# Kernel optimization log

Hardware: AMD Instinct MI355X
Metric: run time of the kernel (lower is better)

## Reference

```python
import jax, jax.numpy as jnp
import numpy as np

N_PTS0 = 32      # n_sampling_points
N_PTS1 = 8       # n_final_points after maxpool
DIM_LOI = 128    # hardcoded via reshape(128, ...) in LinePooling
DIM_FC = 1024
N_LABELS = 3
C_IN = 256
H = W = 128
N_LINES = 16000


def setup_inputs() -> dict:
    key = jax.random.key(0)
    ks = jax.random.split(key, 8)
    features = jax.random.normal(ks[0], (1, C_IN, H, W), jnp.float32)
    # line endpoints (x1,y1,x2,y2) in feature-map coordinates [0, 128)
    lines = jax.random.uniform(ks[1], (N_LINES, 4), jnp.float32) * 128.0
    w_fc1 = jax.random.normal(ks[2], (DIM_LOI, C_IN), jnp.float32) / np.sqrt(C_IN)
    b_fc1 = jnp.zeros((DIM_LOI,), jnp.float32)
    w1 = jax.random.normal(ks[3], (DIM_FC, DIM_LOI * N_PTS1), jnp.float32) / np.sqrt(DIM_LOI * N_PTS1)
    b1 = jnp.zeros((DIM_FC,), jnp.float32)
    w2 = jax.random.normal(ks[4], (DIM_FC, DIM_FC), jnp.float32) / np.sqrt(DIM_FC)
    b2 = jnp.zeros((DIM_FC,), jnp.float32)
    w3 = jax.random.normal(ks[5], (N_LABELS, DIM_FC), jnp.float32) / np.sqrt(DIM_FC)
    b3 = jnp.zeros((N_LABELS,), jnp.float32)
    return {"features": features, "lines": lines, "w_fc1": w_fc1, "b_fc1": b_fc1,
            "w1": w1, "b1": b1, "w2": w2, "b2": b2, "w3": w3, "b3": b3}


def _line_pool(loi, lines):
    # loi: [C, H, W]; lines: [N, 4] -> pooled features [N, C * N_PTS1]
    h, w = loi.shape[1], loi.shape[2]
    tspan = jnp.linspace(0.0, 1.0, N_PTS0)[None, None, :]          # [1,1,S]
    U, V = lines[:, :2], lines[:, 2:]                               # [N,2]
    pts = U[:, :, None] * tspan + V[:, :, None] * (1.0 - tspan) - 0.5  # [N,2,S]
    pts = pts.transpose(0, 2, 1).reshape(-1, 2)                     # [N*S,2]
    px, py = pts[:, 0], pts[:, 1]
    px0 = jnp.clip(jnp.floor(px), 0.0, w - 1)
    py0 = jnp.clip(jnp.floor(py), 0.0, h - 1)
    px1 = jnp.clip(px0 + 1.0, 0.0, w - 1)
    py1 = jnp.clip(py0 + 1.0, 0.0, h - 1)
    px0l, py0l = px0.astype(jnp.int32), py0.astype(jnp.int32)
    px1l, py1l = px1.astype(jnp.int32), py1.astype(jnp.int32)
    # four-corner bilinear gather: each gather is [C, N*S]
    xp = (loi[:, py0l, px0l] * (py1 - py) * (px1 - px)
          + loi[:, py1l, px0l] * (py - py0) * (px1 - px)
          + loi[:, py0l, px1l] * (py1 - py) * (px - px0)
          + loi[:, py1l, px1l] * (py - py0) * (px - px0))
    xp = xp.reshape(DIM_LOI, -1, N_PTS0).transpose(1, 0, 2)         # [N,C,S]
    k = N_PTS0 // N_PTS1
    xp = xp.reshape(xp.shape[0], DIM_LOI, N_PTS1, k).max(axis=-1)   # maxpool1d
    return xp.reshape(-1, N_PTS1 * DIM_LOI)                         # [N, C*P1]


def reference(features, lines, w_fc1, b_fc1, w1, b1, w2, b2, w3, b3):
    # fc1: 1x1 conv 256 -> 128 + ReLU (batch = 1)
    loi = jax.nn.relu(jnp.einsum('oc,chw->ohw', w_fc1, features[0]) + b_fc1[:, None, None])
    feat = _line_pool(loi, lines)                                   # [N, 1024]
    x = jax.nn.relu(feat @ w1.T + b1)
    x = jax.nn.relu(x @ w2.T + b2)
    logits = x @ w3.T + b3                                          # [N, N_LABELS]
    return logits
```

## Files before the change

### kernel.cpp

```cpp
#include <hip/hip_runtime.h>
#include <hip/hip_bf16.h>
#include <math.h>

#define C_IN 256
#define HW 128
#define NPIX (HW*HW)
#define DIM_LOI 128
#define N_LINES 16000
#define N_PTS0 32
#define N_PTS1 8
#define DIM_FC 1024
#define N_LABELS 3

typedef __attribute__((ext_vector_type(8))) short short8;
typedef __attribute__((ext_vector_type(4))) float f32x4;

__global__ __launch_bounds__(256) void transpose_feats(
    const float* __restrict__ feats,
    __hip_bfloat16* __restrict__ featsT)
{
    __shared__ float tile[64][65];
    const int t = threadIdx.x;
    const int p0 = blockIdx.x * 64;
    const int c0 = blockIdx.y * 64;
#pragma unroll
    for (int i = 0; i < 4; ++i) {
        int c = (t >> 4) + i * 16;
        int p4 = (t & 15) * 4;
        float4 v = *(const float4*)(feats + (size_t)(c0 + c) * NPIX + p0 + p4);
        tile[c][p4 + 0] = v.x;
        tile[c][p4 + 1] = v.y;
        tile[c][p4 + 2] = v.z;
        tile[c][p4 + 3] = v.w;
    }
    __syncthreads();
#pragma unroll
    for (int i = 0; i < 2; ++i) {
        int p = (t >> 3) + i * 32;
        int cc = (t & 7) * 8;
        union { __hip_bfloat16 h[8]; uint4 u4; } pk;
#pragma unroll
        for (int j = 0; j < 8; ++j) pk.h[j] = __float2bfloat16(tile[cc + j][p]);
        *(uint4*)(featsT + (size_t)(p0 + p) * C_IN + c0 + cc) = pk.u4;
    }
}

__global__ __launch_bounds__(256) void pool_kernel(
    const __hip_bfloat16* __restrict__ loi,
    const float* __restrict__ lines,
    __hip_bfloat16* __restrict__ feat)
{
    __shared__ int   offs[4][N_PTS0][4];
    __shared__ float wts[4][N_PTS0][4];
    const int g = threadIdx.x >> 6;
    const int t = threadIdx.x & 63;
    const int l = blockIdx.x * 4 + g;

    if (t < N_PTS0) {
        int j = t;
        float tt = (float)j * (1.0f / 31.0f);
        float U0 = lines[4 * l + 0], U1 = lines[4 * l + 1];
        float V0 = lines[4 * l + 2], V1 = lines[4 * l + 3];
        float px = U0 * tt + V0 * (1.0f - tt) - 0.5f;
        float py = U1 * tt + V1 * (1.0f - tt) - 0.5f;
        float px0 = fminf(fmaxf(floorf(px), 0.0f), 127.0f);
        float py0 = fminf(fmaxf(floorf(py), 0.0f), 127.0f);
        float px1 = fminf(fmaxf(px0 + 1.0f, 0.0f), 127.0f);
        float py1 = fminf(fmaxf(py0 + 1.0f, 0.0f), 127.0f);
        int ix0 = (int)px0, iy0 = (int)py0, ix1 = (int)px1, iy1 = (int)py1;
        float wx0 = px1 - px, wx1 = px - px0;
        float wy0 = py1 - py, wy1 = py - py0;
        offs[g][j][0] = (iy0 * HW + ix0) * 64;
        offs[g][j][1] = (iy1 * HW + ix0) * 64;
        offs[g][j][2] = (iy0 * HW + ix1) * 64;
        offs[g][j][3] = (iy1 * HW + ix1) * 64;
        wts[g][j][0] = wy0 * wx0;
        wts[g][j][1] = wy1 * wx0;
        wts[g][j][2] = wy0 * wx1;
        wts[g][j][3] = wy1 * wx1;
    }
    __syncthreads();

    const unsigned int* loi32 = (const unsigned int*)loi;
    unsigned int* featw = (unsigned int*)(feat + (size_t)l * (N_PTS1 * DIM_LOI));

#pragma unroll
    for (int p = 0; p < N_PTS1; ++p) {
        float b0 = -INFINITY, b1 = -INFINITY;
#pragma unroll
        for (int q = 0; q < 4; ++q) {
            int j = p * 4 + q;
            unsigned int v0 = loi32[offs[g][j][0] + t];
            unsigned int v1 = loi32[offs[g][j][1] + t];
            unsigned int v2 = loi32[offs[g][j][2] + t];
            unsigned int v3 = loi32[offs[g][j][3] + t];
            float w0 = wts[g][j][0], w1 = wts[g][j][1];
            float w2 = wts[g][j][2], w3 = wts[g][j][3];
            float sl = w0 * __uint_as_float(v0 << 16)
                     + w1 * __uint_as_float(v1 << 16)
                     + w2 * __uint_as_float(v2 << 16)
                     + w3 * __uint_as_float(v3 << 16);
            float sh = w0 * __uint_as_float(v0 & 0xffff0000u)
                     + w1 * __uint_as_float(v1 & 0xffff0000u)
                     + w2 * __uint_as_float(v2 & 0xffff0000u)
                     + w3 * __uint_as_float(v3 & 0xffff0000u);
            b0 = fmaxf(b0, sl);
            b1 = fmaxf(b1, sh);
        }
        union { __hip_bfloat16 h[2]; unsigned int u; } pk;
        pk.h[0] = __float2bfloat16(b0);
        pk.h[1] = __float2bfloat16(b1);
        featw[p * 64 + t] = pk.u;
    }
}

__global__ __launch_bounds__(256) void to_bf16(
    const float* __restrict__ src, __hip_bfloat16* __restrict__ dst, int n4)
{
    int i = blockIdx.x * blockDim.x + threadIdx.x;
    if (i < n4) {
        float4 v = *(const float4*)(src + (size_t)i * 4);
        dst[(size_t)i * 4 + 0] = __float2bfloat16(v.x);
        dst[(size_t)i * 4 + 1] = __float2bfloat16(v.y);
        dst[(size_t)i * 4 + 2] = __float2bfloat16(v.z);
        dst[(size_t)i * 4 + 3] = __float2bfloat16(v.w);
    }
}

__global__ __launch_bounds__(256) void permute_w1(
    const float* __restrict__ w1, __hip_bfloat16* __restrict__ w1p)
{
    __shared__ float row[1024];
    const int n = blockIdx.x;
    const int t = threadIdx.x;
    ((float4*)row)[t] = ((const float4*)(w1 + (size_t)n * 1024))[t];
    __syncthreads();
    unsigned int* dst = (unsigned int*)(w1p + (size_t)n * 1024);
#pragma unroll
    for (int pass = 0; pass < 2; ++pass) {
        int j = pass * 256 + t;
        int k0 = 2 * j, k1 = 2 * j + 1;
        float v0 = row[(k0 & 127) * 8 + (k0 >> 7)];
        float v1 = row[(k1 & 127) * 8 + (k1 >> 7)];
        union { __hip_bfloat16 h[2]; unsigned int u; } pk;
        pk.h[0] = __float2bfloat16(v0);
        pk.h[1] = __float2bfloat16(v1);
        dst[j] = pk.u;
    }
}

template <int RELU, typename OutT>
__global__ __launch_bounds__(256) void mfma_gemm(
    const __hip_bfloat16* __restrict__ A,
    const __hip_bfloat16* __restrict__ B,
    const float* __restrict__ bias,
    OutT* __restrict__ out,
    int M, int N, int K, int n_tiles)
{
    __shared__ __hip_bfloat16 As[128 * 64];
    __shared__ __hip_bfloat16 Bs[128 * 64];
    const int tid  = threadIdx.x;
    const int lane = tid & 63;
    const int wave = tid >> 6;
    const int wr = wave >> 1, wc = wave & 1;
    const int quad = lane >> 4;
    const int l16  = lane & 15;

    const int lid = blockIdx.x;
    const int per = gridDim.x >> 3;
    const int g   = (lid & 7) * per + (lid >> 3);
    const int n0 = (g % n_tiles) * 128;
    const int m0 = (g / n_tiles) * 128;

    f32x4 acc[4][4];
#pragma unroll
    for (int i = 0; i < 4; ++i)
#pragma unroll
        for (int j = 0; j < 4; ++j) { f32x4 z = {0.f, 0.f, 0.f, 0.f}; acc[i][j] = z; }

    for (int k0 = 0; k0 < K; k0 += 64) {
#pragma unroll
        for (int s = 0; s < 4; ++s) {
            int li   = s * 256 + tid;
            int row  = (li & 511) >> 2;
            int ke   = (li >> 9) * 32 + (li & 3) * 8;
            const __hip_bfloat16* ga = A + (size_t)(m0 + row) * K + k0 + ke;
            const __hip_bfloat16* gb = B + (size_t)(n0 + row) * K + k0 + ke;
            int chunk = s * 256 + (tid & ~63);
            __builtin_amdgcn_global_load_lds(
                (const __attribute__((address_space(1))) unsigned int*)ga,
                (__attribute__((address_space(3))) unsigned int*)(As + chunk * 8),
                16, 0, 0);
            __builtin_amdgcn_global_load_lds(
                (const __attribute__((address_space(1))) unsigned int*)gb,
                (__attribute__((address_space(3))) unsigned int*)(Bs + chunk * 8),
                16, 0, 0);
        }
        __syncthreads();

#pragma unroll
        for (int kh = 0; kh < 2; ++kh) {
            const short* ap = (const short*)As + kh * 4096;
            const short* bp = (const short*)Bs + kh * 4096;
            short8 af[4], bf[4];
#pragma unroll
            for (int mt = 0; mt < 4; ++mt) {
                int row = wr * 64 + mt * 16 + l16;
                af[mt] = *(const short8*)(ap + row * 32 + quad * 8);
            }
#pragma unroll
            for (int nt = 0; nt < 4; ++nt) {
                int row = wc * 64 + nt * 16 + l16;
                bf[nt] = *(const short8*)(bp + row * 32 + quad * 8);
            }
#pragma unroll
            for (int mt = 0; mt < 4; ++mt)
#pragma unroll
                for (int nt = 0; nt < 4; ++nt)
                    acc[mt][nt] = __builtin_amdgcn_mfma_f32_16x16x32_bf16(
                        af[mt], bf[nt], acc[mt][nt], 0, 0, 0);
        }
        __syncthreads();
    }

#pragma unroll
    for (int nt = 0; nt < 4; ++nt) {
        int n = n0 + wc * 64 + nt * 16 + l16;
        float bv = bias[n];
#pragma unroll
        for (int mt = 0; mt < 4; ++mt) {
            int mbase = m0 + wr * 64 + mt * 16 + quad * 4;
#pragma unroll
            for (int r = 0; r < 4; ++r) {
                float v = acc[mt][nt][r] + bv;
                if (RELU) v = v > 0.0f ? v : 0.0f;
                out[(size_t)(mbase + r) * N + n] = (OutT)v;
            }
        }
    }
}

__global__ __launch_bounds__(256) void head_kernel(
    const __hip_bfloat16* __restrict__ x2,
    const float* __restrict__ w3,
    const float* __restrict__ b3,
    float* __restrict__ out)
{
    const int gtid = blockIdx.x * blockDim.x + threadIdx.x;
    const int l = gtid >> 6;
    const int lane = threadIdx.x & 63;
    if (l >= N_LINES) return;
    const __hip_bfloat16* xr = x2 + (size_t)l * DIM_FC;
    float s0 = 0.0f, s1 = 0.0f, s2 = 0.0f;
#pragma unroll
    for (int it = 0; it < 4; ++it) {
        int k = it * 256 + lane * 4;
        ushort4 xv = *(const ushort4*)(xr + k);
        float x0 = __uint_as_float((unsigned)xv.x << 16);
        float x1 = __uint_as_float((unsigned)xv.y << 16);
        float x2v = __uint_as_float((unsigned)xv.z << 16);
        float x3 = __uint_as_float((unsigned)xv.w << 16);
        float4 wa = *(const float4*)(w3 + 0 * DIM_FC + k);
        float4 wb = *(const float4*)(w3 + 1 * DIM_FC + k);
        float4 wc = *(const float4*)(w3 + 2 * DIM_FC + k);
        s0 += x0 * wa.x + x1 * wa.y + x2v * wa.z + x3 * wa.w;
        s1 += x0 * wb.x + x1 * wb.y + x2v * wb.z + x3 * wb.w;
        s2 += x0 * wc.x + x1 * wc.y + x2v * wc.z + x3 * wc.w;
    }
#pragma unroll
    for (int off = 32; off > 0; off >>= 1) {
        s0 += __shfl_xor(s0, off);
        s1 += __shfl_xor(s1, off);
        s2 += __shfl_xor(s2, off);
    }
    if (lane == 0) {
        out[(size_t)l * 3 + 0] = s0 + b3[0];
        out[(size_t)l * 3 + 1] = s1 + b3[1];
        out[(size_t)l * 3 + 2] = s2 + b3[2];
    }
}

extern "C" void kernel_launch(void* const* d_in, const int* in_sizes, int n_in,
                              void* d_out, int out_size, void* d_ws, size_t ws_size,
                              hipStream_t stream) {
    const float* features = (const float*)d_in[0];
    const float* lines    = (const float*)d_in[1];
    const float* w_fc1    = (const float*)d_in[2];
    const float* b_fc1    = (const float*)d_in[3];
    const float* w1       = (const float*)d_in[4];
    const float* b1       = (const float*)d_in[5];
    const float* w2       = (const float*)d_in[6];
    const float* b2       = (const float*)d_in[7];
    const float* w3       = (const float*)d_in[8];
    const float* b3       = (const float*)d_in[9];
    float* out = (float*)d_out;

    char* ws = (char*)d_ws;
    __hip_bfloat16* loi    = (__hip_bfloat16*)ws;
    __hip_bfloat16* featb  = (__hip_bfloat16*)(ws + (size_t)8 * 1024 * 1024);
    __hip_bfloat16* x1b    = (__hip_bfloat16*)(ws + (size_t)40 * 1024 * 1024);
    __hip_bfloat16* x2b    = featb;
    __hip_bfloat16* w1b    = (__hip_bfloat16*)(ws + (size_t)72 * 1024 * 1024);
    __hip_bfloat16* w2b    = (__hip_bfloat16*)(ws + (size_t)74 * 1024 * 1024);
    __hip_bfloat16* featsT = (__hip_bfloat16*)(ws + (size_t)76 * 1024 * 1024);
    __hip_bfloat16* wfc1b  = (__hip_bfloat16*)(ws + (size_t)84 * 1024 * 1024);

    transpose_feats<<<dim3(NPIX / 64, C_IN / 64), 256, 0, stream>>>(features, featsT);
    to_bf16<<<dim3((DIM_LOI * C_IN / 4 + 255) / 256), 256, 0, stream>>>(w_fc1, wfc1b, DIM_LOI * C_IN / 4);
    permute_w1<<<dim3(DIM_FC), 256, 0, stream>>>(w1, w1b);
    to_bf16<<<dim3((DIM_FC * DIM_FC / 4 + 255) / 256), 256, 0, stream>>>(w2, w2b, DIM_FC * DIM_FC / 4);

    mfma_gemm<1, __hip_bfloat16><<<dim3(NPIX / 128), 256, 0, stream>>>(
        featsT, wfc1b, b_fc1, loi, NPIX, DIM_LOI, C_IN, 1);

    pool_kernel<<<dim3(N_LINES / 4), 256, 0, stream>>>(loi, lines, featb);

    mfma_gemm<1, __hip_bfloat16><<<dim3((N_LINES / 128) * (DIM_FC / 128)), 256, 0, stream>>>(
        featb, w1b, b1, x1b, N_LINES, DIM_FC, DIM_FC, DIM_FC / 128);

    mfma_gemm<1, __hip_bfloat16><<<dim3((N_LINES / 128) * (DIM_FC / 128)), 256, 0, stream>>>(
        x1b, w2b, b2, x2b, N_LINES, DIM_FC, DIM_FC, DIM_FC / 128);

    head_kernel<<<dim3((N_LINES * 64 + 255) / 256), 256, 0, stream>>>(x2b, w3, b3, out);
}
```

Baseline: 226.4 us.

## Fuse final 3-label head into second FC GEMM epilogue via atomics

The second FC GEMM epilogue now applies bias and ReLU, multiplies by the three w3 rows, reduces across lanes, and atomically adds partial logits into an output pre-filled with b3. This removes the x2 bf16 write and reread (about 32 MB) and the separate head kernel launch. In exchange it adds a small init kernel and many float atomics (8 column tiles per row). Summation order is no longer deterministic, and x2 is no longer rounded to bf16.

```diff
diff --git a/kernel.cpp b/kernel.cpp
--- a/kernel.cpp
+++ b/kernel.cpp
@@ -149,13 +149,22 @@
     }
 }
 
-template <int RELU, typename OutT>
+__global__ __launch_bounds__(256) void init_out(
+    const float* __restrict__ b3, float* __restrict__ out)
+{
+    int i = blockIdx.x * 256 + threadIdx.x;
+    if (i < N_LINES * N_LABELS) out[i] = b3[i % 3];
+}
+
+template <int MODE>
 __global__ __launch_bounds__(256) void mfma_gemm(
     const __hip_bfloat16* __restrict__ A,
     const __hip_bfloat16* __restrict__ B,
     const float* __restrict__ bias,
-    OutT* __restrict__ out,
-    int M, int N, int K, int n_tiles)
+    __hip_bfloat16* __restrict__ out,
+    int M, int N, int K, int n_tiles,
+    const float* __restrict__ w3,
+    float* __restrict__ logits)
 {
     __shared__ __hip_bfloat16 As[128 * 64];
     __shared__ __hip_bfloat16 Bs[128 * 64];
@@ -223,60 +232,64 @@
         __syncthreads();
     }
 
-#pragma unroll
-    for (int nt = 0; nt < 4; ++nt) {
-        int n = n0 + wc * 64 + nt * 16 + l16;
-        float bv = bias[n];
+    if (MODE == 0) {
+#pragma unroll
+        for (int nt = 0; nt < 4; ++nt) {
+            int n = n0 + wc * 64 + nt * 16 + l16;
+            float bv = bias[n];
+#pragma unroll
+            for (int mt = 0; mt < 4; ++mt) {
+                int mbase = m0 + wr * 64 + mt * 16 + quad * 4;
+#pragma unroll
+                for (int r = 0; r < 4; ++r) {
+                    float v = acc[mt][nt][r] + bv;
+                    v = v > 0.0f ? v : 0.0f;
+                    out[(size_t)(mbase + r) * N + n] = (__hip_bfloat16)v;
+                }
+            }
+        }
+    } else {
 #pragma unroll
         for (int mt = 0; mt < 4; ++mt) {
-            int mbase = m0 + wr * 64 + mt * 16 + quad * 4;
-#pragma unroll
-            for (int r = 0; r < 4; ++r) {
-                float v = acc[mt][nt][r] + bv;
-                if (RELU) v = v > 0.0f ? v : 0.0f;
-                out[(size_t)(mbase + r) * N + n] = (OutT)v;
-            }
-        }
-    }
-}
-
-__global__ __launch_bounds__(256) void head_kernel(
-    const __hip_bfloat16* __restrict__ x2,
-    const float* __restrict__ w3,
-    const float* __restrict__ b3,
-    float* __restrict__ out)
-{
-    const int gtid = blockIdx.x * blockDim.x + threadIdx.x;
-    const int l = gtid >> 6;
-    const int lane = threadIdx.x & 63;
-    if (l >= N_LINES) return;
-    const __hip_bfloat16* xr = x2 + (size_t)l * DIM_FC;
-    float s0 = 0.0f, s1 = 0.0f, s2 = 0.0f;
-#pragma unroll
-    for (int it = 0; it < 4; ++it) {
-        int k = it * 256 + lane * 4;
-        ushort4 xv = *(const ushort4*)(xr + k);
-        float x0 = __uint_as_float((unsigned)xv.x << 16);
-        float x1 = __uint_as_float((unsigned)xv.y << 16);
-        float x2v = __uint_as_float((unsigned)xv.z << 16);
-        float x3 = __uint_as_float((unsigned)xv.w << 16);
-        float4 wa = *(const float4*)(w3 + 0 * DIM_FC + k);
-        float4 wb = *(const float4*)(w3 + 1 * DIM_FC + k);
-        float4 wc = *(const float4*)(w3 + 2 * DIM_FC + k);
-        s0 += x0 * wa.x + x1 * wa.y + x2v * wa.z + x3 * wa.w;
-        s1 += x0 * wb.x + x1 * wb.y + x2v * wb.z + x3 * wb.w;
-        s2 += x0 * wc.x + x1 * wc.y + x2v * wc.z + x3 * wc.w;
-    }
-#pragma unroll
-    for (int off = 32; off > 0; off >>= 1) {
-        s0 += __shfl_xor(s0, off);
-        s1 += __shfl_xor(s1, off);
-        s2 += __shfl_xor(s2, off);
-    }
-    if (lane == 0) {
-        out[(size_t)l * 3 + 0] = s0 + b3[0];
-        out[(size_t)l * 3 + 1] = s1 + b3[1];
-        out[(size_t)l * 3 + 2] = s2 + b3[2];
+            float s[4][3];
+#pragma unroll
+            for (int r = 0; r < 4; ++r) { s[r][0] = 0.f; s[r][1] = 0.f; s[r][2] = 0.f; }
+#pragma unroll
+            for (int nt = 0; nt < 4; ++nt) {
+                int n = n0 + wc * 64 + nt * 16 + l16;
+                float bv  = bias[n];
+                float w30 = w3[n];
+                float w31 = w3[DIM_FC + n];
+                float w32 = w3[2 * DIM_FC + n];
+#pragma unroll
+                for (int r = 0; r < 4; ++r) {
+                    float v = acc[mt][nt][r] + bv;
+                    v = v > 0.0f ? v : 0.0f;
+                    s[r][0] += v * w30;
+                    s[r][1] += v * w31;
+                    s[r][2] += v * w32;
+                }
+            }
+#pragma unroll
+            for (int r = 0; r < 4; ++r)
+#pragma unroll
+                for (int j = 0; j < 3; ++j) {
+                    float v = s[r][j];
+                    v += __shfl_xor(v, 1);
+                    v += __shfl_xor(v, 2);
+                    v += __shfl_xor(v, 4);
+                    v += __shfl_xor(v, 8);
+                    s[r][j] = v;
+                }
+            if (l16 == 0) {
+                int mbase = m0 + wr * 64 + mt * 16 + quad * 4;
+#pragma unroll
+                for (int r = 0; r < 4; ++r)
+#pragma unroll
+                    for (int j = 0; j < 3; ++j)
+                        atomicAdd(logits + (size_t)(mbase + r) * 3 + j, s[r][j]);
+            }
+        }
     }
 }
 
@@ -299,7 +312,6 @@
     __hip_bfloat16* loi    = (__hip_bfloat16*)ws;
     __hip_bfloat16* featb  = (__hip_bfloat16*)(ws + (size_t)8 * 1024 * 1024);
     __hip_bfloat16* x1b    = (__hip_bfloat16*)(ws + (size_t)40 * 1024 * 1024);
-    __hip_bfloat16* x2b    = featb;
     __hip_bfloat16* w1b    = (__hip_bfloat16*)(ws + (size_t)72 * 1024 * 1024);
     __hip_bfloat16* w2b    = (__hip_bfloat16*)(ws + (size_t)74 * 1024 * 1024);
     __hip_bfloat16* featsT = (__hip_bfloat16*)(ws + (size_t)76 * 1024 * 1024);
@@ -309,17 +321,16 @@
     to_bf16<<<dim3((DIM_LOI * C_IN / 4 + 255) / 256), 256, 0, stream>>>(w_fc1, wfc1b, DIM_LOI * C_IN / 4);
     permute_w1<<<dim3(DIM_FC), 256, 0, stream>>>(w1, w1b);
     to_bf16<<<dim3((DIM_FC * DIM_FC / 4 + 255) / 256), 256, 0, stream>>>(w2, w2b, DIM_FC * DIM_FC / 4);
-
-    mfma_gemm<1, __hip_bfloat16><<<dim3(NPIX / 128), 256, 0, stream>>>(
-        featsT, wfc1b, b_fc1, loi, NPIX, DIM_LOI, C_IN, 1);
+    init_out<<<dim3((N_LINES * N_LABELS + 255) / 256), 256, 0, stream>>>(b3, out);
+
+    mfma_gemm<0><<<dim3(NPIX / 128), 256, 0, stream>>>(
+        featsT, wfc1b, b_fc1, loi, NPIX, DIM_LOI, C_IN, 1, nullptr, nullptr);
 
     pool_kernel<<<dim3(N_LINES / 4), 256, 0, stream>>>(loi, lines, featb);
 
-    mfma_gemm<1, __hip_bfloat16><<<dim3((N_LINES / 128) * (DIM_FC / 128)), 256, 0, stream>>>(
-        featb, w1b, b1, x1b, N_LINES, DIM_FC, DIM_FC, DIM_FC / 128);
-
-    mfma_gemm<1, __hip_bfloat16><<<dim3((N_LINES / 128) * (DIM_FC / 128)), 256, 0, stream>>>(
-        x1b, w2b, b2, x2b, N_LINES, DIM_FC, DIM_FC, DIM_FC / 128);
-
-    head_kernel<<<dim3((N_LINES * 64 + 255) / 256), 256, 0, stream>>>(x2b, w3, b3, out);
-}
+    mfma_gemm<0><<<dim3((N_LINES / 128) * (DIM_FC / 128)), 256, 0, stream>>>(
+        featb, w1b, b1, x1b, N_LINES, DIM_FC, DIM_FC, DIM_FC / 128, nullptr, nullptr);
+
+    mfma_gemm<1><<<dim3((N_LINES / 128) * (DIM_FC / 128)), 256, 0, stream>>>(
+        x1b, w2b, b2, nullptr, N_LINES, DIM_FC, DIM_FC, DIM_FC / 128, w3, out);
+}
```

Measured after the change: 272.5 us. +20.4%, slower.
